# Kernel tuning notes

Measured on AMD Instinct MI355X. Metric: run time of the kernel, lower is better.

Reference implementation:

```python
import jax, jax.numpy as jnp
import numpy as np

EMBED_DIM = 1024
NUM_HEADS = 16
HEAD_DIM = 64


def setup_inputs() -> dict:
    key = jax.random.key(0)
    k_x, k_wqkv, k_bqkv, k_wo, k_bo = jax.random.split(key, 5)
    hd = NUM_HEADS * HEAD_DIM
    x = jax.random.normal(k_x, (2, 2048, EMBED_DIM), dtype=jnp.float32)
    # nn.Linear-style init scale
    s1 = 1.0 / np.sqrt(EMBED_DIM)
    s2 = 1.0 / np.sqrt(hd)
    W_qkv = jax.random.uniform(k_wqkv, (EMBED_DIM, 3 * hd), jnp.float32, -s1, s1)
    b_qkv = jax.random.uniform(k_bqkv, (3 * hd,), jnp.float32, -s1, s1)
    W_out = jax.random.uniform(k_wo, (hd, EMBED_DIM), jnp.float32, -s2, s2)
    b_out = jax.random.uniform(k_bo, (EMBED_DIM,), jnp.float32, -s2, s2)
    return {"x": x, "W_qkv": W_qkv, "b_qkv": b_qkv, "W_out": W_out, "b_out": b_out}


def reference(x, W_qkv, b_qkv, W_out, b_out):
    b, s, _ = x.shape
    h, d = NUM_HEADS, HEAD_DIM
    qkv = x @ W_qkv + b_qkv                      # [b, s, 3*h*d]
    qkv = qkv.reshape(b, s, 3, h, d)             # packed order (three, h, d)
    q, k, v = qkv[:, :, 0], qkv[:, :, 1], qkv[:, :, 2]  # each [b, s, h, d]
    scale = 1.0 / jnp.sqrt(jnp.asarray(d, x.dtype))
    scores = jnp.einsum('bshd,bthd->bhst', q, k) * scale  # [b, h, s, s]
    probs = jax.nn.softmax(scores, axis=-1)
    out = jnp.einsum('bhst,bthd->bshd', probs, v)          # [b, s, h, d]
    out = out.reshape(b, s, h * d)
    return out @ W_out + b_out                   # [b, s, embed_dim]
```

## Files before the change

### kernel.cpp

```cpp
#include <hip/hip_runtime.h>

typedef __attribute__((ext_vector_type(8))) short short8;
typedef __attribute__((ext_vector_type(4))) float f32x4;
typedef unsigned short u16;
typedef unsigned int u32;
typedef unsigned long long u64;

#define EMBED 1024
#define SEQ 2048
#define NH 16
#define HD 64

#define MFMA(a, b, c) __builtin_amdgcn_mfma_f32_16x16x32_bf16(a, b, c, 0, 0, 0)

__device__ __forceinline__ u16 f2bf(float f) {
  union { float f; u32 u; } v; v.f = f;
  u32 r = v.u + 0x7fffu + ((v.u >> 16) & 1u);
  return (u16)(r >> 16);
}

__device__ __forceinline__ u32 cvtpk(float lo, float hi) {
  u32 r;
  asm("v_cvt_pk_bf16_f32 %0, %1, %2" : "=v"(r) : "v"(lo), "v"(hi));
  return r;
}

__device__ __forceinline__ float ex2(float x) { return __builtin_amdgcn_exp2f(x); }

__device__ __forceinline__ void async16(const void* g, void* l) {
  __builtin_amdgcn_global_load_lds(
      (const __attribute__((address_space(1))) void*)(uintptr_t)g,
      (__attribute__((address_space(3))) void*)(u32)(uintptr_t)l, 16, 0, 0);
}

__global__ __launch_bounds__(256) void prep_kernel(
    const float* __restrict__ x, u16* __restrict__ xb,
    const float* __restrict__ Wq, u16* __restrict__ Wqt,
    const float* __restrict__ Wo, u16* __restrict__ Wot) {
  int bx = blockIdx.x;
  if (bx < 4096) {
    int i = bx * 256 + threadIdx.x;
    float4 v = ((const float4*)x)[i];
    u64 pk = (u64)f2bf(v.x) | ((u64)f2bf(v.y) << 16) | ((u64)f2bf(v.z) << 32) |
             ((u64)f2bf(v.w) << 48);
    ((u64*)xb)[i] = pk;
    return;
  }
  __shared__ float tile[32][33];
  const int K = 1024;
  int bx2 = bx - 4096;
  int nb = bx2 & 127, kb = bx2 >> 7;
  const float* W; u16* Wt; int N, n0;
  if (nb < 96) { W = Wq; Wt = Wqt; N = 3072; n0 = nb * 32; }
  else         { W = Wo; Wt = Wot; N = 1024; n0 = (nb - 96) * 32; }
  int k0 = kb * 32;
  int tx = threadIdx.x & 31, ty = threadIdx.x >> 5;
#pragma unroll
  for (int p = 0; p < 4; ++p)
    tile[ty + 8 * p][tx] = W[(u64)(k0 + ty + 8 * p) * N + n0 + tx];
  __syncthreads();
#pragma unroll
  for (int p = 0; p < 4; ++p)
    Wt[(u64)(n0 + ty + 8 * p) * K + k0 + tx] = f2bf(tile[tx][ty + 8 * p]);
}

__global__ __launch_bounds__(256) void gemm_qkv_kernel(
    const u16* __restrict__ A, const u16* __restrict__ Bt, const float* __restrict__ bias,
    u16* __restrict__ qb, u16* __restrict__ kb, u16* __restrict__ vtb) {
  __shared__ u16 As[3][128 * 32];
  __shared__ u16 Bs[3][128 * 32];
  const int K = 1024;
  int bid = blockIdx.x;
  int wg = (bid & 7) * 96 + (bid >> 3);
  int m0 = (wg / 24) * 128, n0 = (wg % 24) * 128;
  int tid = threadIdx.x, w = tid >> 6, lane = tid & 63;
  int wm = w >> 1, wn = w & 1;
  int c = lane & 15, g = lane >> 4;

  f32x4 acc[4][4] = {};

  int srow = lane >> 2;
  int scol = (lane & 3) * 8;
  const u16* a0 = A + (u64)m0 * K;
  const u16* b0 = Bt + (u64)n0 * K;

  auto stage = [&](int buf, int kt) {
#pragma unroll
    for (int i = 0; i < 2; ++i) {
      int chunk = w * 2 + i;
      int row = chunk * 16 + srow;
      async16(a0 + (u64)row * K + kt + scol, (char*)As[buf] + chunk * 1024 + lane * 16);
      async16(b0 + (u64)row * K + kt + scol, (char*)Bs[buf] + chunk * 1024 + lane * 16);
    }
  };

  stage(0, 0);
  stage(1, 32);
#pragma unroll
  for (int it = 0; it < 32; ++it) {
    int cur = it % 3;
    if (it + 2 < 32) {
      stage((it + 2) % 3, (it + 2) * 32);
      asm volatile("s_waitcnt vmcnt(8)" ::: "memory");
    } else if (it + 1 < 32) {
      asm volatile("s_waitcnt vmcnt(4)" ::: "memory");
    } else {
      asm volatile("s_waitcnt vmcnt(0)" ::: "memory");
    }
    __builtin_amdgcn_s_barrier();
    asm volatile("" ::: "memory");
    short8 af[4], bfr[4];
#pragma unroll
    for (int i = 0; i < 4; ++i)
      af[i] = *(const short8*)(As[cur] + (wm * 64 + i * 16 + c) * 32 + g * 8);
#pragma unroll
    for (int j = 0; j < 4; ++j)
      bfr[j] = *(const short8*)(Bs[cur] + (wn * 64 + j * 16 + c) * 32 + g * 8);
#pragma unroll
    for (int i = 0; i < 4; ++i)
#pragma unroll
      for (int j = 0; j < 4; ++j)
        acc[i][j] = MFMA(af[i], bfr[j], acc[i][j]);
    asm volatile("s_waitcnt lgkmcnt(0)" ::: "memory");
    __builtin_amdgcn_s_barrier();
    asm volatile("" ::: "memory");
  }

  const float QSCALE = 0.125f * 1.44269504f;
#pragma unroll
  for (int j = 0; j < 4; ++j) {
    int col = n0 + wn * 64 + j * 16 + c;
    float bv = bias[col];
    int sel = col >> 10;
    int h = (col & 1023) >> 6, d = col & 63;
#pragma unroll
    for (int i = 0; i < 4; ++i) {
      int rowb = m0 + wm * 64 + i * 16 + g * 4;
      int b = rowb >> 11, s = rowb & 2047;
      int bh = b * NH + h;
      if (sel == 0) {
#pragma unroll
        for (int r = 0; r < 4; ++r)
          qb[((u64)bh * SEQ + (s + r)) * HD + d] = f2bf((acc[i][j][r] + bv) * QSCALE);
      } else if (sel == 1) {
#pragma unroll
        for (int r = 0; r < 4; ++r)
          kb[((u64)bh * SEQ + (s + r)) * HD + d] = f2bf(acc[i][j][r] + bv);
      } else {
        u64 pk = 0;
#pragma unroll
        for (int r = 0; r < 4; ++r) pk |= (u64)f2bf(acc[i][j][r] + bv) << (16 * r);
        *(u64*)(vtb + ((u64)bh * HD + d) * SEQ + s) = pk;
      }
    }
  }
}

__global__ __launch_bounds__(256, 2) void attn_kernel(const u16* __restrict__ qb,
                                                      const u16* __restrict__ kb,
                                                      const u16* __restrict__ vtb,
                                                      u16* __restrict__ aout) {
  __shared__ __align__(16) u16 Ks[2][64 * 64];
  __shared__ __align__(16) u16 Vts[2][64 * 64];
  __shared__ __align__(16) u16 Pb[4][32 * 64];
  int bid = blockIdx.x;
  int wg = (bid & 7) * 64 + (bid >> 3);
  int bh = wg >> 4;
  int q0 = (wg & 15) * 128;
  int tid = threadIdx.x, w = tid >> 6, lane = tid & 63;
  int c = lane & 15, g = lane >> 4;

  const u16* Qb = qb + ((u64)bh * SEQ + q0 + w * 32) * HD;
  short8 qf[2][2];
#pragma unroll
  for (int i = 0; i < 2; ++i)
#pragma unroll
    for (int ks = 0; ks < 2; ++ks)
      qf[i][ks] = *(const short8*)(Qb + (i * 16 + c) * HD + ks * 32 + g * 8);

  f32x4 o[2][4] = {};
  f32x4 lacc[2] = {};

  int sr = lane >> 3;
  int se = 8 * ((lane & 7) ^ sr);
  char* Pw = (char*)&Pb[w][0] + c * 128;
  u32 pswz = (c & 7) << 4;
  const u16* kbase = kb + (u64)bh * SEQ * HD;
  const u16* vbase = vtb + (u64)bh * HD * SEQ;

  auto stage = [&](int buf, int t0) {
#pragma unroll
    for (int i = 0; i < 2; ++i) {
      int chunk = w * 2 + i;
      int row = chunk * 8 + sr;
      async16(kbase + (u64)(t0 + row) * HD + se,
              (char*)Ks[buf] + chunk * 1024 + lane * 16);
      async16(vbase + (u64)row * SEQ + t0 + se,
              (char*)Vts[buf] + chunk * 1024 + lane * 16);
    }
  };

  auto body = [&](int cur, int t0, bool last) {
    if (!last) {
      stage(cur ^ 1, t0 + 64);
      asm volatile("s_waitcnt vmcnt(4)" ::: "memory");
    } else {
      asm volatile("s_waitcnt vmcnt(0)" ::: "memory");
    }
    __builtin_amdgcn_s_barrier();
    asm volatile("" ::: "memory");

    const u16* KsC = Ks[cur];
    const u16* VtsC = Vts[cur];

    f32x4 s0[4] = {}, s1[4] = {};
    __builtin_amdgcn_s_setprio(1);
#pragma unroll
    for (int j = 0; j < 4; ++j) {
      int trow = j * 16 + c;
      int sw = (trow & 7) << 4;
#pragma unroll
      for (int ks = 0; ks < 2; ++ks) {
        short8 ak = *(const short8*)((const char*)KsC + trow * 128 +
                                     ((g * 16 + ks * 64) ^ sw));
        s0[j] = MFMA(ak, qf[0][ks], s0[j]);
        s1[j] = MFMA(ak, qf[1][ks], s1[j]);
      }
    }
    __builtin_amdgcn_s_setprio(0);

#pragma unroll
    for (int j = 0; j < 4; ++j)
#pragma unroll
      for (int r = 0; r < 4; ++r) {
        s0[j][r] = ex2(s0[j][r]);
        s1[j][r] = ex2(s1[j][r]);
      }
    lacc[0] += (s0[0] + s0[1]) + (s0[2] + s0[3]);
    lacc[1] += (s1[0] + s1[1]) + (s1[2] + s1[3]);

    {
      u64 a0 = (u64)cvtpk(s0[0][0], s0[0][1]) | ((u64)cvtpk(s0[0][2], s0[0][3]) << 32);
      u64 a1 = (u64)cvtpk(s0[1][0], s0[1][1]) | ((u64)cvtpk(s0[1][2], s0[1][3]) << 32);
      u64 a2 = (u64)cvtpk(s0[2][0], s0[2][1]) | ((u64)cvtpk(s0[2][2], s0[2][3]) << 32);
      u64 a3 = (u64)cvtpk(s0[3][0], s0[3][1]) | ((u64)cvtpk(s0[3][2], s0[3][3]) << 32);
      *(u64*)(Pw + ((g * 8 + 0)  ^ pswz)) = a0;
      *(u64*)(Pw + ((g * 8 + 32) ^ pswz)) = a1;
      *(u64*)(Pw + ((g * 8 + 64) ^ pswz)) = a2;
      *(u64*)(Pw + ((g * 8 + 96) ^ pswz)) = a3;
      u64 b0 = (u64)cvtpk(s1[0][0], s1[0][1]) | ((u64)cvtpk(s1[0][2], s1[0][3]) << 32);
      u64 b1 = (u64)cvtpk(s1[1][0], s1[1][1]) | ((u64)cvtpk(s1[1][2], s1[1][3]) << 32);
      u64 b2 = (u64)cvtpk(s1[2][0], s1[2][1]) | ((u64)cvtpk(s1[2][2], s1[2][3]) << 32);
      u64 b3 = (u64)cvtpk(s1[3][0], s1[3][1]) | ((u64)cvtpk(s1[3][2], s1[3][3]) << 32);
      *(u64*)(Pw + 2048 + ((g * 8 + 0)  ^ pswz)) = b0;
      *(u64*)(Pw + 2048 + ((g * 8 + 32) ^ pswz)) = b1;
      *(u64*)(Pw + 2048 + ((g * 8 + 64) ^ pswz)) = b2;
      *(u64*)(Pw + 2048 + ((g * 8 + 96) ^ pswz)) = b3;
    }

    __builtin_amdgcn_s_setprio(1);
#pragma unroll
    for (int ks = 0; ks < 2; ++ks) {
      short8 pa0 = *(const short8*)(Pw + ((ks * 64 + g * 16) ^ pswz));
      short8 pa1 = *(const short8*)(Pw + 2048 + ((ks * 64 + g * 16) ^ pswz));
#pragma unroll
      for (int jd = 0; jd < 4; ++jd) {
        int drow = jd * 16 + c;
        int sw = (drow & 7) << 4;
        short8 bv = *(const short8*)((const char*)VtsC + drow * 128 +
                                     ((g * 16 + ks * 64) ^ sw));
        o[0][jd] = MFMA(pa0, bv, o[0][jd]);
        o[1][jd] = MFMA(pa1, bv, o[1][jd]);
      }
    }
    __builtin_amdgcn_s_setprio(0);

    asm volatile("s_waitcnt lgkmcnt(0)" ::: "memory");
    __builtin_amdgcn_s_barrier();
    asm volatile("" ::: "memory");
  };

  stage(0, 0);
  const int NT = SEQ / 64;
  for (int it = 0; it < NT; it += 2) {
    body(0, it * 64, false);
    body(1, it * 64 + 64, it + 2 >= NT);
  }

  int hh = bh & 15, b = bh >> 4;
#pragma unroll
  for (int i = 0; i < 2; ++i) {
    float l = (lacc[i][0] + lacc[i][1]) + (lacc[i][2] + lacc[i][3]);
    l += __shfl_xor(l, 16);
    l += __shfl_xor(l, 32);
    float inv = 1.0f / l;
    float invr[4];
#pragma unroll
    for (int r = 0; r < 4; ++r) invr[r] = __shfl(inv, g * 4 + r);
#pragma unroll
    for (int r = 0; r < 4; ++r) {
      int q = q0 + w * 32 + i * 16 + g * 4 + r;
#pragma unroll
      for (int jd = 0; jd < 4; ++jd)
        aout[(u64)(b * SEQ + q) * EMBED + hh * HD + jd * 16 + c] =
            f2bf(o[i][jd][r] * invr[r]);
    }
  }
}

__global__ __launch_bounds__(256) void gemm_out_kernel(const u16* __restrict__ A,
                                                       const u16* __restrict__ Bt,
                                                       const float* __restrict__ bias,
                                                       float* __restrict__ out) {
  __shared__ u16 As[3][128 * 32];
  __shared__ u16 Bs[3][64 * 32];
  const int K = 1024;
  int bid = blockIdx.x;
  int wg = (bid & 7) * 64 + (bid >> 3);
  int m0 = (wg >> 4) * 128, n0 = (wg & 15) * 64;
  int tid = threadIdx.x, w = tid >> 6, lane = tid & 63;
  int wm = w >> 1, wn = w & 1;
  int c = lane & 15, g = lane >> 4;

  f32x4 acc[4][2] = {};
  int srow = lane >> 2;
  int scol = (lane & 3) * 8;
  const u16* a0 = A + (u64)m0 * K;
  const u16* b0 = Bt + (u64)n0 * K;

  auto stage = [&](int buf, int kt) {
#pragma unroll
    for (int i = 0; i < 2; ++i) {
      int chunk = w * 2 + i;
      int row = chunk * 16 + srow;
      async16(a0 + (u64)row * K + kt + scol, (char*)As[buf] + chunk * 1024 + lane * 16);
    }
    int brow = w * 16 + srow;
    async16(b0 + (u64)brow * K + kt + scol, (char*)Bs[buf] + w * 1024 + lane * 16);
  };

  stage(0, 0);
  stage(1, 32);
#pragma unroll
  for (int it = 0; it < 32; ++it) {
    int cur = it % 3;
    if (it + 2 < 32) {
      stage((it + 2) % 3, (it + 2) * 32);
      asm volatile("s_waitcnt vmcnt(6)" ::: "memory");
    } else if (it + 1 < 32) {
      asm volatile("s_waitcnt vmcnt(3)" ::: "memory");
    } else {
      asm volatile("s_waitcnt vmcnt(0)" ::: "memory");
    }
    __builtin_amdgcn_s_barrier();
    asm volatile("" ::: "memory");
    short8 af[4], bfr[2];
#pragma unroll
    for (int i = 0; i < 4; ++i)
      af[i] = *(const short8*)(As[cur] + (wm * 64 + i * 16 + c) * 32 + g * 8);
#pragma unroll
    for (int j = 0; j < 2; ++j)
      bfr[j] = *(const short8*)(Bs[cur] + (wn * 32 + j * 16 + c) * 32 + g * 8);
#pragma unroll
    for (int i = 0; i < 4; ++i)
#pragma unroll
      for (int j = 0; j < 2; ++j)
        acc[i][j] = MFMA(af[i], bfr[j], acc[i][j]);
    asm volatile("s_waitcnt lgkmcnt(0)" ::: "memory");
    __builtin_amdgcn_s_barrier();
    asm volatile("" ::: "memory");
  }

#pragma unroll
  for (int j = 0; j < 2; ++j) {
    int col = n0 + wn * 32 + j * 16 + c;
    float bv = bias[col];
#pragma unroll
    for (int i = 0; i < 4; ++i) {
      int rowb = m0 + wm * 64 + i * 16 + g * 4;
#pragma unroll
      for (int r = 0; r < 4; ++r)
        out[(u64)(rowb + r) * EMBED + col] = acc[i][j][r] + bv;
    }
  }
}

extern "C" void kernel_launch(void* const* d_in, const int* in_sizes, int n_in,
                              void* d_out, int out_size, void* d_ws, size_t ws_size,
                              hipStream_t stream) {
  const float* x = (const float*)d_in[0];
  const float* Wqkv = (const float*)d_in[1];
  const float* bqkv = (const float*)d_in[2];
  const float* Wout = (const float*)d_in[3];
  const float* bout = (const float*)d_in[4];
  float* out = (float*)d_out;
  char* ws = (char*)d_ws;

  u16* xb  = (u16*)(ws);
  u16* wqt = (u16*)(ws + (8ull << 20));
  u16* wot = (u16*)(ws + (14ull << 20));
  u16* qb  = (u16*)(ws + (16ull << 20));
  u16* kb  = (u16*)(ws + (24ull << 20));
  u16* vtb = (u16*)(ws + (32ull << 20));
  u16* aout = xb;

  prep_kernel<<<dim3(8192), dim3(256), 0, stream>>>(x, xb, Wqkv, wqt, Wout, wot);
  gemm_qkv_kernel<<<dim3(768), dim3(256), 0, stream>>>(xb, wqt, bqkv, qb, kb, vtb);
  attn_kernel<<<dim3(512), dim3(256), 0, stream>>>(qb, kb, vtb, aout);
  gemm_out_kernel<<<dim3(512), dim3(256), 0, stream>>>(aout, wot, bout, out);
}
```

Before: 108.4 us.

## Use two waves per attention block, each handling 64 query rows

The attention kernel now launches 128-thread blocks with two waves, and each wave processes four 16-row query groups instead of two. Each K/V fragment read from LDS is therefore reused across twice as many MFMAs, which cuts LDS read traffic per FLOP and halves the number of waves staging K/V tiles. The cost is much higher register pressure (doubled accumulators and Q fragments) and fewer waves per block to hide latency. The launch_bounds min-blocks hint is also dropped.

```diff
diff --git a/kernel.cpp b/kernel.cpp
--- a/kernel.cpp
+++ b/kernel.cpp
@@ -156,13 +156,13 @@
   }
 }
 
-__global__ __launch_bounds__(256, 2) void attn_kernel(const u16* __restrict__ qb,
-                                                      const u16* __restrict__ kb,
-                                                      const u16* __restrict__ vtb,
-                                                      u16* __restrict__ aout) {
+__global__ __launch_bounds__(128) void attn_kernel(const u16* __restrict__ qb,
+                                                   const u16* __restrict__ kb,
+                                                   const u16* __restrict__ vtb,
+                                                   u16* __restrict__ aout) {
   __shared__ __align__(16) u16 Ks[2][64 * 64];
   __shared__ __align__(16) u16 Vts[2][64 * 64];
-  __shared__ __align__(16) u16 Pb[4][32 * 64];
+  __shared__ __align__(16) u16 Pb[2][64 * 64];
   int bid = blockIdx.x;
   int wg = (bid & 7) * 64 + (bid >> 3);
   int bh = wg >> 4;
@@ -170,16 +170,16 @@
   int tid = threadIdx.x, w = tid >> 6, lane = tid & 63;
   int c = lane & 15, g = lane >> 4;
 
-  const u16* Qb = qb + ((u64)bh * SEQ + q0 + w * 32) * HD;
-  short8 qf[2][2];
-#pragma unroll
-  for (int i = 0; i < 2; ++i)
+  const u16* Qb = qb + ((u64)bh * SEQ + q0 + w * 64) * HD;
+  short8 qf[4][2];
+#pragma unroll
+  for (int i = 0; i < 4; ++i)
 #pragma unroll
     for (int ks = 0; ks < 2; ++ks)
       qf[i][ks] = *(const short8*)(Qb + (i * 16 + c) * HD + ks * 32 + g * 8);
 
-  f32x4 o[2][4] = {};
-  f32x4 lacc[2] = {};
+  f32x4 o[4][4] = {};
+  f32x4 lacc[4] = {};
 
   int sr = lane >> 3;
   int se = 8 * ((lane & 7) ^ sr);
@@ -190,8 +190,8 @@
 
   auto stage = [&](int buf, int t0) {
 #pragma unroll
-    for (int i = 0; i < 2; ++i) {
-      int chunk = w * 2 + i;
+    for (int i = 0; i < 4; ++i) {
+      int chunk = w * 4 + i;
       int row = chunk * 8 + sr;
       async16(kbase + (u64)(t0 + row) * HD + se,
               (char*)Ks[buf] + chunk * 1024 + lane * 16);
@@ -203,7 +203,7 @@
   auto body = [&](int cur, int t0, bool last) {
     if (!last) {
       stage(cur ^ 1, t0 + 64);
-      asm volatile("s_waitcnt vmcnt(4)" ::: "memory");
+      asm volatile("s_waitcnt vmcnt(8)" ::: "memory");
     } else {
       asm volatile("s_waitcnt vmcnt(0)" ::: "memory");
     }
@@ -213,7 +213,7 @@
     const u16* KsC = Ks[cur];
     const u16* VtsC = Vts[cur];
 
-    f32x4 s0[4] = {}, s1[4] = {};
+    f32x4 s[4][4] = {};
     __builtin_amdgcn_s_setprio(1);
 #pragma unroll
     for (int j = 0; j < 4; ++j) {
@@ -223,54 +223,50 @@
       for (int ks = 0; ks < 2; ++ks) {
         short8 ak = *(const short8*)((const char*)KsC + trow * 128 +
                                      ((g * 16 + ks * 64) ^ sw));
-        s0[j] = MFMA(ak, qf[0][ks], s0[j]);
-        s1[j] = MFMA(ak, qf[1][ks], s1[j]);
+#pragma unroll
+        for (int grp = 0; grp < 4; ++grp)
+          s[grp][j] = MFMA(ak, qf[grp][ks], s[grp][j]);
       }
     }
     __builtin_amdgcn_s_setprio(0);
 
 #pragma unroll
-    for (int j = 0; j < 4; ++j)
-#pragma unroll
-      for (int r = 0; r < 4; ++r) {
-        s0[j][r] = ex2(s0[j][r]);
-        s1[j][r] = ex2(s1[j][r]);
+    for (int grp = 0; grp < 4; ++grp) {
+#pragma unroll
+      for (int j = 0; j < 4; ++j)
+#pragma unroll
+        for (int r = 0; r < 4; ++r)
+          s[grp][j][r] = ex2(s[grp][j][r]);
+      lacc[grp] += (s[grp][0] + s[grp][1]) + (s[grp][2] + s[grp][3]);
+    }
+
+#pragma unroll
+    for (int grp = 0; grp < 4; ++grp) {
+      char* pb = Pw + grp * 2048;
+#pragma unroll
+      for (int j = 0; j < 4; ++j) {
+        u64 pk = (u64)cvtpk(s[grp][j][0], s[grp][j][1]) |
+                 ((u64)cvtpk(s[grp][j][2], s[grp][j][3]) << 32);
+        *(u64*)(pb + ((g * 8 + j * 32) ^ pswz)) = pk;
       }
-    lacc[0] += (s0[0] + s0[1]) + (s0[2] + s0[3]);
-    lacc[1] += (s1[0] + s1[1]) + (s1[2] + s1[3]);
-
-    {
-      u64 a0 = (u64)cvtpk(s0[0][0], s0[0][1]) | ((u64)cvtpk(s0[0][2], s0[0][3]) << 32);
-      u64 a1 = (u64)cvtpk(s0[1][0], s0[1][1]) | ((u64)cvtpk(s0[1][2], s0[1][3]) << 32);
-      u64 a2 = (u64)cvtpk(s0[2][0], s0[2][1]) | ((u64)cvtpk(s0[2][2], s0[2][3]) << 32);
-      u64 a3 = (u64)cvtpk(s0[3][0], s0[3][1]) | ((u64)cvtpk(s0[3][2], s0[3][3]) << 32);
-      *(u64*)(Pw + ((g * 8 + 0)  ^ pswz)) = a0;
-      *(u64*)(Pw + ((g * 8 + 32) ^ pswz)) = a1;
-      *(u64*)(Pw + ((g * 8 + 64) ^ pswz)) = a2;
-      *(u64*)(Pw + ((g * 8 + 96) ^ pswz)) = a3;
-      u64 b0 = (u64)cvtpk(s1[0][0], s1[0][1]) | ((u64)cvtpk(s1[0][2], s1[0][3]) << 32);
-      u64 b1 = (u64)cvtpk(s1[1][0], s1[1][1]) | ((u64)cvtpk(s1[1][2], s1[1][3]) << 32);
-      u64 b2 = (u64)cvtpk(s1[2][0], s1[2][1]) | ((u64)cvtpk(s1[2][2], s1[2][3]) << 32);
-      u64 b3 = (u64)cvtpk(s1[3][0], s1[3][1]) | ((u64)cvtpk(s1[3][2], s1[3][3]) << 32);
-      *(u64*)(Pw + 2048 + ((g * 8 + 0)  ^ pswz)) = b0;
-      *(u64*)(Pw + 2048 + ((g * 8 + 32) ^ pswz)) = b1;
-      *(u64*)(Pw + 2048 + ((g * 8 + 64) ^ pswz)) = b2;
-      *(u64*)(Pw + 2048 + ((g * 8 + 96) ^ pswz)) = b3;
     }
 
     __builtin_amdgcn_s_setprio(1);
 #pragma unroll
     for (int ks = 0; ks < 2; ++ks) {
-      short8 pa0 = *(const short8*)(Pw + ((ks * 64 + g * 16) ^ pswz));
-      short8 pa1 = *(const short8*)(Pw + 2048 + ((ks * 64 + g * 16) ^ pswz));
+      short8 pa[4];
+#pragma unroll
+      for (int grp = 0; grp < 4; ++grp)
+        pa[grp] = *(const short8*)(Pw + grp * 2048 + ((ks * 64 + g * 16) ^ pswz));
 #pragma unroll
       for (int jd = 0; jd < 4; ++jd) {
         int drow = jd * 16 + c;
         int sw = (drow & 7) << 4;
         short8 bv = *(const short8*)((const char*)VtsC + drow * 128 +
                                      ((g * 16 + ks * 64) ^ sw));
-        o[0][jd] = MFMA(pa0, bv, o[0][jd]);
-        o[1][jd] = MFMA(pa1, bv, o[1][jd]);
+#pragma unroll
+        for (int grp = 0; grp < 4; ++grp)
+          o[grp][jd] = MFMA(pa[grp], bv, o[grp][jd]);
       }
     }
     __builtin_amdgcn_s_setprio(0);
@@ -289,7 +285,7 @@
 
   int hh = bh & 15, b = bh >> 4;
 #pragma unroll
-  for (int i = 0; i < 2; ++i) {
+  for (int i = 0; i < 4; ++i) {
     float l = (lacc[i][0] + lacc[i][1]) + (lacc[i][2] + lacc[i][3]);
     l += __shfl_xor(l, 16);
     l += __shfl_xor(l, 32);
@@ -299,7 +295,7 @@
     for (int r = 0; r < 4; ++r) invr[r] = __shfl(inv, g * 4 + r);
 #pragma unroll
     for (int r = 0; r < 4; ++r) {
-      int q = q0 + w * 32 + i * 16 + g * 4 + r;
+      int q = q0 + w * 64 + i * 16 + g * 4 + r;
 #pragma unroll
       for (int jd = 0; jd < 4; ++jd)
         aout[(u64)(b * SEQ + q) * EMBED + hh * HD + jd * 16 + c] =
@@ -406,6 +402,6 @@
 
   prep_kernel<<<dim3(8192), dim3(256), 0, stream>>>(x, xb, Wqkv, wqt, Wout, wot);
   gemm_qkv_kernel<<<dim3(768), dim3(256), 0, stream>>>(xb, wqt, bqkv, qb, kb, vtb);
-  attn_kernel<<<dim3(512), dim3(256), 0, stream>>>(qb, kb, vtb, aout);
+  attn_kernel<<<dim3(512), dim3(128), 0, stream>>>(qb, kb, vtb, aout);
   gemm_out_kernel<<<dim3(512), dim3(256), 0, stream>>>(aout, wot, bout, out);
 }
```

New measurement: 122.1 us. +12.6%, slower.
